# Kernel tuning notes

Hardware: AMD Instinct MI355X
Metric: run time of the kernel (lower is better)

## Reference

```python
import jax, jax.numpy as jnp
import numpy as np

MAX_DISP = 4  # PWC-Net correlation: displacements in [-4,4] -> 9x9 = 81 channels


def setup_inputs() -> dict:
    key = jax.random.key(0)
    k1, k2 = jax.random.split(key)
    B, C, H, W = 8, 128, 112, 192
    tensorFirst = jax.random.normal(k1, (B, C, H, W), dtype=jnp.float32)
    tensorSecond = jax.random.normal(k2, (B, C, H, W), dtype=jnp.float32)
    return {"tensorFirst": tensorFirst, "tensorSecond": tensorSecond}


def reference(tensorFirst, tensorSecond):
    B, C, H, W = tensorFirst.shape
    D = MAX_DISP
    # zero-pad second by max displacement on each spatial side (rbot padding of 8 = 2*4)
    padded = jnp.pad(tensorSecond, ((0, 0), (0, 0), (D, D), (D, D)))
    outs = []
    # fixed 9x9 displacement grid; channel index = (dy+4)*9 + (dx+4)
    for dy in range(2 * D + 1):
        for dx in range(2 * D + 1):
            shifted = jax.lax.dynamic_slice(padded, (0, 0, dy, dx), (B, C, H, W))
            # dot product over channels, normalized by C (sumelems in the cupy kernel)
            outs.append(jnp.mean(tensorFirst * shifted, axis=1))
    return jnp.stack(outs, axis=1)  # [B, 81, H, W]
```

## Files before the change

kernel.cpp:

```cpp
#include <hip/hip_runtime.h>


namespace {
constexpr int kC = 128;
constexpr int kH = 112;
constexpr int kW = 192;
constexpr int kD = 4;
constexpr int kKD = 9;
constexpr int kHW = kH * kW;
constexpr long long kCHW = (long long)kC * kHW;

constexpr int PX = 8;
constexpr int XG = kW / PX;
constexpr int YT = 8;
constexpr int NT = XG * YT;
constexpr int TILE = YT * kW;
}

__device__ __attribute__((aligned(16))) float g_zero_row[kW] = {};

typedef const __attribute__((address_space(1))) void* gas_ptr;
typedef __attribute__((address_space(3))) void* las_ptr;

__device__ __forceinline__ void gload16(const float* g, float* l) {
  __builtin_amdgcn_global_load_lds((gas_ptr)g, (las_ptr)l, 16, 0, 0);
}

__global__ __launch_bounds__(NT, 4)
void corr81_kernel(const float* __restrict__ first,
                   const float* __restrict__ second,
                   float* __restrict__ out) {
  __shared__ __align__(16) float zpad[4];
  __shared__ __align__(16) float Sb[2][TILE];
  __shared__ __align__(16) float Fb[2][TILE];

  const int g = blockIdx.x;
  const int b = g & 7;
  const int i = g >> 3;
  const int dy = i % kKD;
  const int y0 = (i / kKD) * YT;

  const int tid = threadIdx.x;
  const int xg = tid % XG;
  const int yl = tid / XG;
  const int px0 = xg * PX;
  const int ys0 = y0 + dy - kD;

  if (tid == 0) { zpad[0] = 0.f; zpad[1] = 0.f; zpad[2] = 0.f; zpad[3] = 0.f; }

  const float* fsrc = first + (long long)b * kCHW + (long long)y0 * kW +
                      (long long)tid * 4;
  const float* ssrc[2];
  long long sstr[2];
#pragma unroll
  for (int j = 0; j < 2; ++j) {
    const int pos = j * NT + tid;
    const int r = pos / 48;
    const int col4 = (pos - r * 48) * 4;
    const int ysr = ys0 + r;
    const bool inb = (unsigned)ysr < (unsigned)kH;
    ssrc[j] = inb ? (second + (long long)b * kCHW + (long long)ysr * kW + col4)
                  : (g_zero_row + col4);
    sstr[j] = inb ? (long long)kHW : 0ll;
  }

  float acc[PX][kKD];
#pragma unroll
  for (int p = 0; p < PX; ++p)
#pragma unroll
    for (int d = 0; d < kKD; ++d) acc[p][d] = 0.0f;

  auto stage = [&](int P) {
    gload16(fsrc,            &Fb[P][tid * 4]);
    gload16(fsrc + NT * 4,   &Fb[P][tid * 4 + NT * 4]);
    gload16(ssrc[0],         &Sb[P][tid * 4]);
    gload16(ssrc[1],         &Sb[P][tid * 4 + NT * 4]);
    fsrc += kHW;
    ssrc[0] += sstr[0];
    ssrc[1] += sstr[1];
  };

  auto compute = [&](int P) {
    const float* fp = &Fb[P][yl * kW + px0];
    const float* s1 = &Sb[P][yl * kW + px0];
    const float* w0p = (xg == 0) ? zpad : (s1 - 4);
    const float* w3p = (xg == XG - 1) ? zpad : (s1 + 8);
    const float4 f0 = *(const float4*)(fp);
    const float4 f1 = *(const float4*)(fp + 4);
    const float4 w0 = *(const float4*)(w0p);
    const float4 w1 = *(const float4*)(s1);
    const float4 w2 = *(const float4*)(s1 + 4);
    const float4 w3 = *(const float4*)(w3p);

    const float fa[PX] = {f0.x, f0.y, f0.z, f0.w, f1.x, f1.y, f1.z, f1.w};
    const float sw[16] = {w0.x, w0.y, w0.z, w0.w, w1.x, w1.y, w1.z, w1.w,
                          w2.x, w2.y, w2.z, w2.w, w3.x, w3.y, w3.z, w3.w};
#pragma unroll
    for (int p = 0; p < PX; ++p)
#pragma unroll
      for (int d = 0; d < kKD; ++d)
        acc[p][d] = fmaf(fa[p], sw[p + d], acc[p][d]);
  };

  stage(0);
  __syncthreads();
  for (int c = 0; c < kC; c += 2) {
    stage(1);
    compute(0);
    __syncthreads();
    if (c + 2 < kC) stage(0);
    compute(1);
    __syncthreads();
  }

  const float scale = 1.0f / (float)kC;
  float* obase = out + ((long long)b * 81 + (long long)dy * kKD) * kHW +
                 (long long)(y0 + yl) * kW + px0;
#pragma unroll
  for (int d = 0; d < kKD; ++d) {
    float4 o0 = make_float4(acc[0][d] * scale, acc[1][d] * scale,
                            acc[2][d] * scale, acc[3][d] * scale);
    float4 o1 = make_float4(acc[4][d] * scale, acc[5][d] * scale,
                            acc[6][d] * scale, acc[7][d] * scale);
    float* op = obase + (long long)d * kHW;
    *(float4*)op = o0;
    *(float4*)(op + 4) = o1;
  }
}

extern "C" void kernel_launch(void* const* d_in, const int* in_sizes, int n_in,
                              void* d_out, int out_size, void* d_ws, size_t ws_size,
                              hipStream_t stream) {
  const float* first = (const float*)d_in[0];
  const float* second = (const float*)d_in[1];
  float* out = (float*)d_out;

  const int grid = 8 * (kH / YT) * kKD;
  corr81_kernel<<<grid, NT, 0, stream>>>(first, second, out);
}
```

Before: 283.5 us.

## Halve per-thread pixel tile and load first tensor directly into registers

```diff
diff --git a/kernel.cpp b/kernel.cpp
--- a/kernel.cpp
+++ b/kernel.cpp
@@ -10,7 +10,7 @@
 constexpr int kHW = kH * kW;
 constexpr long long kCHW = (long long)kC * kHW;
 
-constexpr int PX = 8;
+constexpr int PX = 4;
 constexpr int XG = kW / PX;
 constexpr int YT = 8;
 constexpr int NT = XG * YT;
@@ -26,13 +26,12 @@
   __builtin_amdgcn_global_load_lds((gas_ptr)g, (las_ptr)l, 16, 0, 0);
 }
 
-__global__ __launch_bounds__(NT, 4)
+__global__ __launch_bounds__(NT, 6)
 void corr81_kernel(const float* __restrict__ first,
                    const float* __restrict__ second,
                    float* __restrict__ out) {
   __shared__ __align__(16) float zpad[4];
   __shared__ __align__(16) float Sb[2][TILE];
-  __shared__ __align__(16) float Fb[2][TILE];
 
   const int g = blockIdx.x;
   const int b = g & 7;
@@ -48,21 +47,19 @@
 
   if (tid == 0) { zpad[0] = 0.f; zpad[1] = 0.f; zpad[2] = 0.f; zpad[3] = 0.f; }
 
-  const float* fsrc = first + (long long)b * kCHW + (long long)y0 * kW +
-                      (long long)tid * 4;
-  const float* ssrc[2];
-  long long sstr[2];
-#pragma unroll
-  for (int j = 0; j < 2; ++j) {
-    const int pos = j * NT + tid;
-    const int r = pos / 48;
-    const int col4 = (pos - r * 48) * 4;
+  const float* ssrc;
+  long long sstr;
+  {
+    const int r = tid / XG;
+    const int col = (tid % XG) * PX;
     const int ysr = ys0 + r;
     const bool inb = (unsigned)ysr < (unsigned)kH;
-    ssrc[j] = inb ? (second + (long long)b * kCHW + (long long)ysr * kW + col4)
-                  : (g_zero_row + col4);
-    sstr[j] = inb ? (long long)kHW : 0ll;
+    ssrc = inb ? (second + (long long)b * kCHW + (long long)ysr * kW + col)
+               : (g_zero_row + col);
+    sstr = inb ? (long long)kHW : 0ll;
   }
+
+  const float* fp = first + (long long)b * kCHW + (long long)(y0 + yl) * kW + px0;
 
   float acc[PX][kKD];
 #pragma unroll
@@ -70,31 +67,24 @@
 #pragma unroll
     for (int d = 0; d < kKD; ++d) acc[p][d] = 0.0f;
 
+  const float* s1p[2] = {&Sb[0][yl * kW + px0], &Sb[1][yl * kW + px0]};
+  const float* w0p[2] = {(xg == 0) ? zpad : s1p[0] - PX,
+                         (xg == 0) ? zpad : s1p[1] - PX};
+  const float* w2p[2] = {(xg == XG - 1) ? zpad : s1p[0] + PX,
+                         (xg == XG - 1) ? zpad : s1p[1] + PX};
+
   auto stage = [&](int P) {
-    gload16(fsrc,            &Fb[P][tid * 4]);
-    gload16(fsrc + NT * 4,   &Fb[P][tid * 4 + NT * 4]);
-    gload16(ssrc[0],         &Sb[P][tid * 4]);
-    gload16(ssrc[1],         &Sb[P][tid * 4 + NT * 4]);
-    fsrc += kHW;
-    ssrc[0] += sstr[0];
-    ssrc[1] += sstr[1];
+    gload16(ssrc, &Sb[P][tid * PX]);
+    ssrc += sstr;
   };
 
-  auto compute = [&](int P) {
-    const float* fp = &Fb[P][yl * kW + px0];
-    const float* s1 = &Sb[P][yl * kW + px0];
-    const float* w0p = (xg == 0) ? zpad : (s1 - 4);
-    const float* w3p = (xg == XG - 1) ? zpad : (s1 + 8);
-    const float4 f0 = *(const float4*)(fp);
-    const float4 f1 = *(const float4*)(fp + 4);
-    const float4 w0 = *(const float4*)(w0p);
-    const float4 w1 = *(const float4*)(s1);
-    const float4 w2 = *(const float4*)(s1 + 4);
-    const float4 w3 = *(const float4*)(w3p);
-
-    const float fa[PX] = {f0.x, f0.y, f0.z, f0.w, f1.x, f1.y, f1.z, f1.w};
-    const float sw[16] = {w0.x, w0.y, w0.z, w0.w, w1.x, w1.y, w1.z, w1.w,
-                          w2.x, w2.y, w2.z, w2.w, w3.x, w3.y, w3.z, w3.w};
+  auto compute = [&](int P, const float4& f) {
+    const float4 w0 = *(const float4*)(w0p[P]);
+    const float4 w1 = *(const float4*)(s1p[P]);
+    const float4 w2 = *(const float4*)(w2p[P]);
+    const float fa[PX] = {f.x, f.y, f.z, f.w};
+    const float sw[12] = {w0.x, w0.y, w0.z, w0.w, w1.x, w1.y, w1.z, w1.w,
+                          w2.x, w2.y, w2.z, w2.w};
 #pragma unroll
     for (int p = 0; p < PX; ++p)
 #pragma unroll
@@ -102,14 +92,20 @@
         acc[p][d] = fmaf(fa[p], sw[p + d], acc[p][d]);
   };
 
+  float4 fcur, fnext;
   stage(0);
+  fcur = *(const float4*)fp; fp += kHW;
   __syncthreads();
   for (int c = 0; c < kC; c += 2) {
     stage(1);
-    compute(0);
+    fnext = *(const float4*)fp; fp += kHW;
+    compute(0, fcur);
     __syncthreads();
-    if (c + 2 < kC) stage(0);
-    compute(1);
+    if (c + 2 < kC) {
+      stage(0);
+      fcur = *(const float4*)fp; fp += kHW;
+    }
+    compute(1, fnext);
     __syncthreads();
   }
 
@@ -118,13 +114,9 @@
                  (long long)(y0 + yl) * kW + px0;
 #pragma unroll
   for (int d = 0; d < kKD; ++d) {
-    float4 o0 = make_float4(acc[0][d] * scale, acc[1][d] * scale,
-                            acc[2][d] * scale, acc[3][d] * scale);
-    float4 o1 = make_float4(acc[4][d] * scale, acc[5][d] * scale,
-                            acc[6][d] * scale, acc[7][d] * scale);
-    float* op = obase + (long long)d * kHW;
-    *(float4*)op = o0;
-    *(float4*)(op + 4) = o1;
+    float4 o = make_float4(acc[0][d] * scale, acc[1][d] * scale,
+                           acc[2][d] * scale, acc[3][d] * scale);
+    *(float4*)(obase + (long long)d * kHW) = o;
   }
 }
 
```

After: 355.6 us. +25.5%, slower.
